# Kernel optimization log

Measured on AMD Instinct MI355X. Metric: run time of the kernel, lower is better.

The kernel has to match this reference:

```python
import jax, jax.numpy as jnp
import numpy as np

# Static problem dims (all graphs equal-sized so adaptive pool = uniform bins)
B = 64          # graphs
N = 2048        # nodes per graph
E = 16          # node_emb_dim
H_OUT, W_OUT = 32, 4   # AdaptiveAvgPool2d output -> pooled_dim = 128
COND = 64       # cond_emb_dim
HID = 512       # mlp_h_dim
BN_EPS = 1e-5


def _lin_init(key, out_d, in_d):
    kw, kb = jax.random.split(key)
    lim = 1.0 / np.sqrt(in_d)
    W = jax.random.uniform(kw, (out_d, in_d), jnp.float32, -lim, lim)
    b = jax.random.uniform(kb, (out_d,), jnp.float32, -lim, lim)
    return W, b


def setup_inputs() -> dict:
    key = jax.random.key(0)
    ks = jax.random.split(key, 6)
    Ntot = B * N
    x = jax.random.normal(ks[0], (Ntot, E), jnp.float32)
    batch = jnp.repeat(jnp.arange(B, dtype=jnp.int32), N)  # sorted segment ids
    cond = jax.random.normal(ks[1], (Ntot, COND), jnp.float32)
    mlp_in = COND + H_OUT * W_OUT  # 192
    W1, b1 = _lin_init(ks[2], HID, mlp_in)
    W2, b2 = _lin_init(ks[3], HID, HID)
    W3, b3 = _lin_init(ks[4], 3, HID)
    g1 = jnp.ones((HID,), jnp.float32); be1 = jnp.zeros((HID,), jnp.float32)
    g2 = jnp.ones((HID,), jnp.float32); be2 = jnp.zeros((HID,), jnp.float32)
    return {"x": x, "batch": batch, "conditioner_z_ref": cond,
            "W1": W1, "b1": b1, "g1": g1, "be1": be1,
            "W2": W2, "b2": b2, "g2": g2, "be2": be2,
            "W3": W3, "b3": b3}


def _bn_gelu(h, g, be):
    # BatchNorm1d in training mode: biased batch stats over the node axis
    m = h.mean(axis=0)
    v = h.var(axis=0)
    h = g * (h - m) * jax.lax.rsqrt(v + BN_EPS) + be
    return jax.nn.gelu(h, approximate=False)


def reference(x, batch, conditioner_z_ref, W1, b1, g1, be1, W2, b2, g2, be2, W3, b3):
    # Per-graph adaptive avg pool: since N % H_OUT == 0 and E % W_OUT == 0,
    # AdaptiveAvgPool2d is exactly mean over uniform (N/H_OUT, E/W_OUT) bins.
    xb = x.reshape(B, H_OUT, N // H_OUT, W_OUT, E // W_OUT)
    batch_pooled = xb.mean(axis=(2, 4)).reshape(B, H_OUT * W_OUT)  # [B, 128]
    pooled_per_node = batch_pooled[batch]                           # gather to [Ntot, 128]
    h = jnp.concatenate([conditioner_z_ref, pooled_per_node], axis=1)  # [Ntot, 192]
    h = _bn_gelu(h @ W1.T + b1, g1, be1)
    h = _bn_gelu(h @ W2.T + b2, g2, be2)
    return h @ W3.T + b3  # [Ntot, 3] predicted coords
```

## Files before the change

kernel.cpp:

```cpp
#include <hip/hip_runtime.h>
#include <hip/hip_bf16.h>
#include <math.h>
#include <stdint.h>

#define B_GRAPHS 64
#define N_NODES  2048
#define E_DIM    16
#define M_TOT    (B_GRAPHS * N_NODES)
#define K_COND   64
#define MLP_IN   192
#define HID      512
#define POOLD    128
#define BN_EPS   1e-5f

typedef __attribute__((ext_vector_type(8))) short bfrag8;
typedef __attribute__((ext_vector_type(4))) float facc4;

__device__ __forceinline__ unsigned short f2b(float f) {
    unsigned int x = __builtin_bit_cast(unsigned int, f);
    unsigned int r = x + 0x7fffu + ((x >> 16) & 1u);
    return (unsigned short)(r >> 16);
}
__device__ __forceinline__ float b2f(unsigned short u) {
    unsigned int x = ((unsigned int)u) << 16;
    return __builtin_bit_cast(float, x);
}

__device__ __forceinline__ float gelu_fast(float y) {
    float x  = y * 0.70710678118654752440f;
    float ax = fabsf(x);
    float t  = __builtin_amdgcn_rcpf(fmaf(0.3275911f, ax, 1.0f));
    float p  = fmaf(1.061405429f, t, -1.453152027f);
    p = fmaf(p, t, 1.421413741f);
    p = fmaf(p, t, -0.284496736f);
    p = fmaf(p, t, 0.254829592f);
    p = p * t;
    float e = __expf(-x * x);
    float erfax = fmaf(-p, e, 1.0f);
    float erfx  = copysignf(erfax, x);
    return 0.5f * y * (1.0f + erfx);
}

#define GLOAD_LDS16(g, l)                                                        \
    __builtin_amdgcn_global_load_lds(                                            \
        (const __attribute__((address_space(1))) unsigned int*)(const void*)(g), \
        (__attribute__((address_space(3))) unsigned int*)(void*)(l), 16, 0, 0)

__global__ __launch_bounds__(512) void prep_kernel(const float* __restrict__ x,
                                                   const float* __restrict__ W1,
                                                   const float* __restrict__ b1,
                                                   float* __restrict__ gbias) {
    __shared__ float pl[POOLD];
    int g = blockIdx.x, t = threadIdx.x;
    if (t < 128) {
        int h = t >> 2, w = t & 3;
        const float* base = x + (size_t)g * N_NODES * E_DIM + (size_t)h * 64 * E_DIM + w * 4;
        float s = 0.f;
        #pragma unroll 4
        for (int r = 0; r < 64; ++r) {
            float4 v = *reinterpret_cast<const float4*>(base + (size_t)r * E_DIM);
            s += v.x + v.y + v.z + v.w;
        }
        pl[h * 4 + w] = s * (1.0f / 256.0f);
    }
    __syncthreads();
    const float* wr_ = W1 + (size_t)t * MLP_IN + K_COND;
    float s = b1[t];
    #pragma unroll 4
    for (int k = 0; k < POOLD; ++k) s = fmaf(pl[k], wr_[k], s);
    gbias[g * HID + t] = s;
}

__global__ __launch_bounds__(256) void cvt_kernel(const float* __restrict__ s,
                                                  unsigned short* __restrict__ d) {
    size_t i = ((size_t)blockIdx.x * 256 + threadIdx.x) * 8;
    float4 v0 = *reinterpret_cast<const float4*>(s + i);
    float4 v1 = *reinterpret_cast<const float4*>(s + i + 4);
    unsigned short t[8] = {f2b(v0.x), f2b(v0.y), f2b(v0.z), f2b(v0.w),
                           f2b(v1.x), f2b(v1.y), f2b(v1.z), f2b(v1.w)};
    *reinterpret_cast<bfrag8*>(d + i) = *reinterpret_cast<bfrag8*>(t);
}

__device__ __forceinline__ bfrag8 load_f32x8_as_bf16(const float* p) {
    float4 v0 = *reinterpret_cast<const float4*>(p);
    float4 v1 = *reinterpret_cast<const float4*>(p + 4);
    unsigned short t[8] = {f2b(v0.x), f2b(v0.y), f2b(v0.z), f2b(v0.w),
                           f2b(v1.x), f2b(v1.y), f2b(v1.z), f2b(v1.w)};
    return *reinterpret_cast<bfrag8*>(t);
}

__global__ __launch_bounds__(256) void gemm1_kernel(const float* __restrict__ A,
                                                    const float* __restrict__ W,
                                                    const int* __restrict__ batch,
                                                    const float* __restrict__ gbias,
                                                    float* __restrict__ sums,
                                                    unsigned short* __restrict__ C) {
    __shared__ float sArr[128], qArr[128];
    const int t = threadIdx.x;
    const int r0 = blockIdx.x * 128, c0 = blockIdx.y * 128;
    const int l = t & 63, w = t >> 6;
    const int wr = w >> 1, wc = w & 1;
    const int ln = l & 15, kg = l >> 4;
    if (t < 128) { sArr[t] = 0.f; qArr[t] = 0.f; }
    __syncthreads();

    facc4 acc[4][4];
    const facc4 z = {0.f, 0.f, 0.f, 0.f};
    #pragma unroll
    for (int a = 0; a < 4; ++a)
        #pragma unroll
        for (int b = 0; b < 4; ++b) acc[a][b] = z;

    #pragma unroll
    for (int ks = 0; ks < 2; ++ks) {
        bfrag8 af[4], bf[4];
        #pragma unroll
        for (int a = 0; a < 4; ++a)
            af[a] = load_f32x8_as_bf16(A + (size_t)(r0 + wr * 64 + a * 16 + ln) * K_COND + ks * 32 + kg * 8);
        #pragma unroll
        for (int b = 0; b < 4; ++b)
            bf[b] = load_f32x8_as_bf16(W + (size_t)(c0 + wc * 64 + b * 16 + ln) * MLP_IN + ks * 32 + kg * 8);
        #pragma unroll
        for (int a = 0; a < 4; ++a)
            #pragma unroll
            for (int b = 0; b < 4; ++b)
                acc[a][b] = __builtin_amdgcn_mfma_f32_16x16x32_bf16(af[a], bf[b], acc[a][b], 0, 0, 0);
    }

    float cs[4] = {0.f, 0.f, 0.f, 0.f}, cq[4] = {0.f, 0.f, 0.f, 0.f};
    #pragma unroll
    for (int a = 0; a < 4; ++a) {
        #pragma unroll
        for (int i = 0; i < 4; ++i) {
            int row = r0 + wr * 64 + a * 16 + kg * 4 + i;
            const float* gb = gbias + (size_t)batch[row] * HID;
            size_t rbase = (size_t)row * HID + c0 + wc * 64 + ln;
            #pragma unroll
            for (int b = 0; b < 4; ++b) {
                float v = acc[a][b][i] + gb[c0 + wc * 64 + b * 16 + ln];
                C[rbase + b * 16] = f2b(v);
                cs[b] += v; cq[b] = fmaf(v, v, cq[b]);
            }
        }
    }
    #pragma unroll
    for (int b = 0; b < 4; ++b) {
        cs[b] += __shfl_xor(cs[b], 16, 64); cq[b] += __shfl_xor(cq[b], 16, 64);
        cs[b] += __shfl_xor(cs[b], 32, 64); cq[b] += __shfl_xor(cq[b], 32, 64);
    }
    if (kg == 0) {
        #pragma unroll
        for (int b = 0; b < 4; ++b) {
            int cl = wc * 64 + b * 16 + ln;
            atomicAdd(&sArr[cl], cs[b]); atomicAdd(&qArr[cl], cq[b]);
        }
    }
    __syncthreads();
    if (t < 128) {
        atomicAdd(&sums[c0 + t], sArr[t]);
        atomicAdd(&sums[HID + c0 + t], qArr[t]);
    }
}

__global__ __launch_bounds__(512, 2) void gemm2_kernel(const unsigned short* __restrict__ A,
                                                       const unsigned short* __restrict__ Bm,
                                                       const float* __restrict__ sums1,
                                                       const float* __restrict__ g1,
                                                       const float* __restrict__ be1,
                                                       const float* __restrict__ bias,
                                                       float* __restrict__ sums,
                                                       unsigned short* __restrict__ C) {
    __shared__ unsigned short As[2][128 * 32];
    __shared__ unsigned short Bs[2][512 * 32];
    __shared__ float lss[2 * HID];
    __shared__ float sArr[HID], qArr[HID];
    const int t = threadIdx.x;
    const int r0 = blockIdx.x * 128;
    const int l = t & 63, w = t >> 6;
    const int wr = w >> 2, wc = w & 3;
    const int ln = l & 15, kg = l >> 4;
    const int arow = t >> 2, aslot = t & 3;
    const int awslot = aslot ^ ((arow >> 1) & 3);
    const int rr = l >> 2, sp = l & 3;
    const int bss = sp ^ ((rr >> 1) & 3);

    {
        float mean = sums1[t] * (1.0f / M_TOT);
        float var  = sums1[HID + t] * (1.0f / M_TOT) - mean * mean;
        float sc   = g1[t] * rsqrtf(var + BN_EPS);
        lss[t] = sc;
        lss[HID + t] = be1[t] - mean * sc;
    }
    sArr[t] = 0.f; qArr[t] = 0.f;

    facc4 acc[4][8];
    const facc4 z = {0.f, 0.f, 0.f, 0.f};
    #pragma unroll
    for (int a = 0; a < 4; ++a)
        #pragma unroll
        for (int b = 0; b < 8; ++b) acc[a][b] = z;

    const unsigned short* aptr = A + (size_t)(r0 + arow) * HID + aslot * 8;
    __syncthreads();

    bfrag8 va_pending;
    {
        bfrag8 va0 = *reinterpret_cast<const bfrag8*>(aptr);
        unsigned short tmp[8];
        #pragma unroll
        for (int j = 0; j < 8; ++j) {
            int col = aslot * 8 + j;
            float xv = b2f((unsigned short)va0[j]);
            tmp[j] = f2b(gelu_fast(fmaf(xv, lss[col], lss[HID + col])));
        }
        *reinterpret_cast<bfrag8*>(&As[0][arow * 32 + awslot * 8]) = *reinterpret_cast<bfrag8*>(tmp);
        #pragma unroll
        for (int c = 0; c < 4; ++c) {
            int chunk = w * 4 + c;
            const unsigned short* gb = Bm + (size_t)(chunk * 16 + rr) * HID + bss * 8;
            GLOAD_LDS16(gb, &Bs[0][chunk * 512]);
        }
        va_pending = *reinterpret_cast<const bfrag8*>(aptr + 32);
    }
    __syncthreads();

    #pragma unroll 2
    for (int step = 0; step < 16; ++step) {
        const int cur = step & 1, nxt = cur ^ 1;
        bfrag8 af[4], bf[8];
        #pragma unroll
        for (int a = 0; a < 4; ++a) {
            int RA = wr * 64 + a * 16 + ln;
            af[a] = *reinterpret_cast<const bfrag8*>(&As[cur][RA * 32 + (kg ^ ((RA >> 1) & 3)) * 8]);
        }
        #pragma unroll
        for (int b = 0; b < 8; ++b) {
            int RB = wc * 128 + b * 16 + ln;
            bf[b] = *reinterpret_cast<const bfrag8*>(&Bs[cur][RB * 32 + (kg ^ ((RB >> 1) & 3)) * 8]);
        }
        if (step < 15) {
            const int kk = (step + 1) * 32;
            #pragma unroll
            for (int c = 0; c < 4; ++c) {
                int chunk = w * 4 + c;
                const unsigned short* gb = Bm + (size_t)(chunk * 16 + rr) * HID + kk + bss * 8;
                GLOAD_LDS16(gb, &Bs[nxt][chunk * 512]);
            }
        }
        bfrag8 va_future;
        if (step < 14) va_future = *reinterpret_cast<const bfrag8*>(aptr + (step + 2) * 32);
        #pragma unroll
        for (int a = 0; a < 4; ++a)
            #pragma unroll
            for (int b = 0; b < 8; ++b)
                acc[a][b] = __builtin_amdgcn_mfma_f32_16x16x32_bf16(af[a], bf[b], acc[a][b], 0, 0, 0);
        if (step < 15) {
            const int kk = (step + 1) * 32;
            unsigned short tmp[8];
            #pragma unroll
            for (int j = 0; j < 8; ++j) {
                int col = kk + aslot * 8 + j;
                float xv = b2f((unsigned short)va_pending[j]);
                tmp[j] = f2b(gelu_fast(fmaf(xv, lss[col], lss[HID + col])));
            }
            *reinterpret_cast<bfrag8*>(&As[nxt][arow * 32 + awslot * 8]) = *reinterpret_cast<bfrag8*>(tmp);
        }
        va_pending = va_future;
        __syncthreads();
    }

    float bb[8];
    #pragma unroll
    for (int b = 0; b < 8; ++b) bb[b] = bias[wc * 128 + b * 16 + ln];
    float cs[8], cq[8];
    #pragma unroll
    for (int b = 0; b < 8; ++b) { cs[b] = 0.f; cq[b] = 0.f; }
    #pragma unroll
    for (int a = 0; a < 4; ++a) {
        #pragma unroll
        for (int i = 0; i < 4; ++i) {
            size_t rbase = (size_t)(r0 + wr * 64 + a * 16 + kg * 4 + i) * HID + wc * 128 + ln;
            #pragma unroll
            for (int b = 0; b < 8; ++b) {
                float v = acc[a][b][i] + bb[b];
                C[rbase + b * 16] = f2b(v);
                cs[b] += v; cq[b] = fmaf(v, v, cq[b]);
            }
        }
    }
    #pragma unroll
    for (int b = 0; b < 8; ++b) {
        cs[b] += __shfl_xor(cs[b], 16, 64); cq[b] += __shfl_xor(cq[b], 16, 64);
        cs[b] += __shfl_xor(cs[b], 32, 64); cq[b] += __shfl_xor(cq[b], 32, 64);
    }
    if (kg == 0) {
        #pragma unroll
        for (int b = 0; b < 8; ++b) {
            int cl = wc * 128 + b * 16 + ln;
            atomicAdd(&sArr[cl], cs[b]); atomicAdd(&qArr[cl], cq[b]);
        }
    }
    __syncthreads();
    atomicAdd(&sums[t], sArr[t]);
    atomicAdd(&sums[HID + t], qArr[t]);
}

__global__ void finalize_kernel(const float* __restrict__ sums, const float* __restrict__ g,
                                const float* __restrict__ be, float* __restrict__ ss) {
    int n = threadIdx.x;
    float mean = sums[n] * (1.0f / M_TOT);
    float var = sums[HID + n] * (1.0f / M_TOT) - mean * mean;
    float sc = g[n] * rsqrtf(var + BN_EPS);
    ss[n] = sc;
    ss[HID + n] = be[n] - mean * sc;
}

__global__ __launch_bounds__(256) void g3_kernel(const unsigned short* __restrict__ H2,
                                                 const float* __restrict__ ss2,
                                                 const float* __restrict__ W3,
                                                 const float* __restrict__ b3,
                                                 float* __restrict__ out) {
    __shared__ float lss[2 * HID];
    __shared__ float lw3[3 * HID];
    int t = threadIdx.x;
    for (int i = t; i < 2 * HID; i += 256) lss[i] = ss2[i];
    for (int i = t; i < 3 * HID; i += 256) lw3[i] = W3[i];
    __syncthreads();
    int l = t & 63, w = t >> 6;
    int rsub = l >> 3, lk = l & 7;
    int row = blockIdx.x * 32 + w * 8 + rsub;
    const unsigned short* p = H2 + (size_t)row * HID;
    float o0 = 0.f, o1 = 0.f, o2 = 0.f;
    #pragma unroll
    for (int it = 0; it < 8; ++it) {
        int k = it * 64 + lk * 8;
        bfrag8 v = *reinterpret_cast<const bfrag8*>(p + k);
        #pragma unroll
        for (int j = 0; j < 8; ++j) {
            float x = b2f((unsigned short)v[j]);
            float y = fmaf(x, lss[k + j], lss[HID + k + j]);
            y = gelu_fast(y);
            o0 = fmaf(y, lw3[k + j], o0);
            o1 = fmaf(y, lw3[HID + k + j], o1);
            o2 = fmaf(y, lw3[2 * HID + k + j], o2);
        }
    }
    #pragma unroll
    for (int m = 1; m < 8; m <<= 1) {
        o0 += __shfl_xor(o0, m, 64);
        o1 += __shfl_xor(o1, m, 64);
        o2 += __shfl_xor(o2, m, 64);
    }
    if (lk == 0) {
        out[(size_t)row * 3 + 0] = o0 + b3[0];
        out[(size_t)row * 3 + 1] = o1 + b3[1];
        out[(size_t)row * 3 + 2] = o2 + b3[2];
    }
}

extern "C" void kernel_launch(void* const* d_in, const int* in_sizes, int n_in,
                              void* d_out, int out_size, void* d_ws, size_t ws_size,
                              hipStream_t stream) {
    const float* x     = (const float*)d_in[0];
    const int*   batch = (const int*)d_in[1];
    const float* cond  = (const float*)d_in[2];
    const float* W1    = (const float*)d_in[3];
    const float* b1    = (const float*)d_in[4];
    const float* g1    = (const float*)d_in[5];
    const float* be1   = (const float*)d_in[6];
    const float* W2    = (const float*)d_in[7];
    const float* b2    = (const float*)d_in[8];
    const float* g2    = (const float*)d_in[9];
    const float* be2   = (const float*)d_in[10];
    const float* W3    = (const float*)d_in[11];
    const float* b3    = (const float*)d_in[12];

    const size_t H_BYTES = (size_t)M_TOT * HID * 2;
    if (ws_size < 2 * H_BYTES) return;
    char* ws = (char*)d_ws;
    unsigned short* H1 = (unsigned short*)ws;
    unsigned short* H2 = (unsigned short*)(ws + H_BYTES);

    float* outf   = (float*)d_out;
    float* gbias  = outf;
    float* sums1  = gbias + B_GRAPHS * HID;
    float* sums2  = sums1 + 2 * HID;
    unsigned short* W2bf = (unsigned short*)(sums2 + 2 * HID);
    float* ss2 = (float*)ws;

    hipMemsetAsync(sums1, 0, 2 * 2 * HID * sizeof(float), stream);

    prep_kernel<<<B_GRAPHS, 512, 0, stream>>>(x, W1, b1, gbias);
    cvt_kernel<<<(HID * HID / 8) / 256, 256, 0, stream>>>(W2, W2bf);

    gemm1_kernel<<<dim3(M_TOT / 128, HID / 128), 256, 0, stream>>>(
        cond, W1, batch, gbias, sums1, H1);

    gemm2_kernel<<<dim3(M_TOT / 128, 1), 512, 0, stream>>>(
        H1, W2bf, sums1, g1, be1, b2, sums2, H2);

    finalize_kernel<<<1, HID, 0, stream>>>(sums2, g2, be2, ss2);

    g3_kernel<<<M_TOT / 32, 256, 0, stream>>>(H2, ss2, W3, b3, outf);
}
```

Baseline: 313.3 us.

## Widen gemm1 tiles to full width and deepen gemm2 prefetch pipeline

gemm1 now has each 512-thread block compute all 512 output columns for its 128 rows. The graph index is derived from the row offset instead of reading the batch array per row, and the per-graph bias is hoisted into registers. gemm2's main loop is rebuilt as a two-stage-ahead pipeline with explicit vmcnt/lgkmcnt waits, raw s_barriers and sched_barriers, so B-tile loads overlap MFMA work better. This relies on the uniform sorted batch layout and adds register pressure in gemm1.

```diff
diff --git a/kernel.cpp b/kernel.cpp
--- a/kernel.cpp
+++ b/kernel.cpp
@@ -89,77 +89,79 @@
     return *reinterpret_cast<bfrag8*>(t);
 }
 
-__global__ __launch_bounds__(256) void gemm1_kernel(const float* __restrict__ A,
-                                                    const float* __restrict__ W,
-                                                    const int* __restrict__ batch,
-                                                    const float* __restrict__ gbias,
-                                                    float* __restrict__ sums,
-                                                    unsigned short* __restrict__ C) {
-    __shared__ float sArr[128], qArr[128];
+__global__ __launch_bounds__(512, 2) void gemm1_kernel(const float* __restrict__ A,
+                                                       const float* __restrict__ W,
+                                                       const float* __restrict__ gbias,
+                                                       float* __restrict__ sums,
+                                                       unsigned short* __restrict__ C) {
+    __shared__ float sArr[HID], qArr[HID];
     const int t = threadIdx.x;
-    const int r0 = blockIdx.x * 128, c0 = blockIdx.y * 128;
+    const int r0 = blockIdx.x * 128;
+    const int g = r0 >> 11;
     const int l = t & 63, w = t >> 6;
-    const int wr = w >> 1, wc = w & 1;
+    const int wr = w >> 2, wc = w & 3;
     const int ln = l & 15, kg = l >> 4;
-    if (t < 128) { sArr[t] = 0.f; qArr[t] = 0.f; }
-    __syncthreads();
-
-    facc4 acc[4][4];
+    sArr[t] = 0.f; qArr[t] = 0.f;
+    __syncthreads();
+
+    facc4 acc[4][8];
     const facc4 z = {0.f, 0.f, 0.f, 0.f};
     #pragma unroll
     for (int a = 0; a < 4; ++a)
         #pragma unroll
-        for (int b = 0; b < 4; ++b) acc[a][b] = z;
+        for (int b = 0; b < 8; ++b) acc[a][b] = z;
 
     #pragma unroll
     for (int ks = 0; ks < 2; ++ks) {
-        bfrag8 af[4], bf[4];
+        bfrag8 af[4], bf[8];
         #pragma unroll
         for (int a = 0; a < 4; ++a)
             af[a] = load_f32x8_as_bf16(A + (size_t)(r0 + wr * 64 + a * 16 + ln) * K_COND + ks * 32 + kg * 8);
         #pragma unroll
-        for (int b = 0; b < 4; ++b)
-            bf[b] = load_f32x8_as_bf16(W + (size_t)(c0 + wc * 64 + b * 16 + ln) * MLP_IN + ks * 32 + kg * 8);
+        for (int b = 0; b < 8; ++b)
+            bf[b] = load_f32x8_as_bf16(W + (size_t)(wc * 128 + b * 16 + ln) * MLP_IN + ks * 32 + kg * 8);
         #pragma unroll
         for (int a = 0; a < 4; ++a)
             #pragma unroll
-            for (int b = 0; b < 4; ++b)
+            for (int b = 0; b < 8; ++b)
                 acc[a][b] = __builtin_amdgcn_mfma_f32_16x16x32_bf16(af[a], bf[b], acc[a][b], 0, 0, 0);
     }
 
-    float cs[4] = {0.f, 0.f, 0.f, 0.f}, cq[4] = {0.f, 0.f, 0.f, 0.f};
+    const float* gb = gbias + (size_t)g * HID;
+    float gbv[8];
+    #pragma unroll
+    for (int b = 0; b < 8; ++b) gbv[b] = gb[wc * 128 + b * 16 + ln];
+    float cs[8], cq[8];
+    #pragma unroll
+    for (int b = 0; b < 8; ++b) { cs[b] = 0.f; cq[b] = 0.f; }
     #pragma unroll
     for (int a = 0; a < 4; ++a) {
         #pragma unroll
         for (int i = 0; i < 4; ++i) {
-            int row = r0 + wr * 64 + a * 16 + kg * 4 + i;
-            const float* gb = gbias + (size_t)batch[row] * HID;
-            size_t rbase = (size_t)row * HID + c0 + wc * 64 + ln;
+            size_t rbase = (size_t)(r0 + wr * 64 + a * 16 + kg * 4 + i) * HID + wc * 128 + ln;
             #pragma unroll
-            for (int b = 0; b < 4; ++b) {
-                float v = acc[a][b][i] + gb[c0 + wc * 64 + b * 16 + ln];
+            for (int b = 0; b < 8; ++b) {
+                float v = acc[a][b][i] + gbv[b];
                 C[rbase + b * 16] = f2b(v);
                 cs[b] += v; cq[b] = fmaf(v, v, cq[b]);
             }
         }
     }
     #pragma unroll
-    for (int b = 0; b < 4; ++b) {
+    for (int b = 0; b < 8; ++b) {
         cs[b] += __shfl_xor(cs[b], 16, 64); cq[b] += __shfl_xor(cq[b], 16, 64);
         cs[b] += __shfl_xor(cs[b], 32, 64); cq[b] += __shfl_xor(cq[b], 32, 64);
     }
     if (kg == 0) {
         #pragma unroll
-        for (int b = 0; b < 4; ++b) {
-            int cl = wc * 64 + b * 16 + ln;
+        for (int b = 0; b < 8; ++b) {
+            int cl = wc * 128 + b * 16 + ln;
             atomicAdd(&sArr[cl], cs[b]); atomicAdd(&qArr[cl], cq[b]);
         }
     }
     __syncthreads();
-    if (t < 128) {
-        atomicAdd(&sums[c0 + t], sArr[t]);
-        atomicAdd(&sums[HID + c0 + t], qArr[t]);
-    }
+    atomicAdd(&sums[t], sArr[t]);
+    atomicAdd(&sums[HID + t], qArr[t]);
 }
 
 __global__ __launch_bounds__(512, 2) void gemm2_kernel(const unsigned short* __restrict__ A,
@@ -201,72 +203,92 @@
         for (int b = 0; b < 8; ++b) acc[a][b] = z;
 
     const unsigned short* aptr = A + (size_t)(r0 + arow) * HID + aslot * 8;
-    __syncthreads();
-
-    bfrag8 va_pending;
-    {
-        bfrag8 va0 = *reinterpret_cast<const bfrag8*>(aptr);
+
+    auto actwrite = [&](bfrag8 va, int kk, int buf) {
         unsigned short tmp[8];
         #pragma unroll
         for (int j = 0; j < 8; ++j) {
-            int col = aslot * 8 + j;
-            float xv = b2f((unsigned short)va0[j]);
+            int col = kk + aslot * 8 + j;
+            float xv = b2f((unsigned short)va[j]);
             tmp[j] = f2b(gelu_fast(fmaf(xv, lss[col], lss[HID + col])));
         }
-        *reinterpret_cast<bfrag8*>(&As[0][arow * 32 + awslot * 8]) = *reinterpret_cast<bfrag8*>(tmp);
+        *reinterpret_cast<bfrag8*>(&As[buf][arow * 32 + awslot * 8]) = *reinterpret_cast<bfrag8*>(tmp);
+    };
+    auto stageB = [&](int kk, int buf) {
         #pragma unroll
         for (int c = 0; c < 4; ++c) {
             int chunk = w * 4 + c;
-            const unsigned short* gb = Bm + (size_t)(chunk * 16 + rr) * HID + bss * 8;
-            GLOAD_LDS16(gb, &Bs[0][chunk * 512]);
-        }
-        va_pending = *reinterpret_cast<const bfrag8*>(aptr + 32);
-    }
-    __syncthreads();
-
-    #pragma unroll 2
-    for (int step = 0; step < 16; ++step) {
-        const int cur = step & 1, nxt = cur ^ 1;
-        bfrag8 af[4], bf[8];
+            const unsigned short* gb = Bm + (size_t)(chunk * 16 + rr) * HID + kk + bss * 8;
+            GLOAD_LDS16(gb, &Bs[buf][chunk * 512]);
+        }
+    };
+    auto dsread = [&](bfrag8* af, bfrag8* bf, int buf) {
         #pragma unroll
         for (int a = 0; a < 4; ++a) {
             int RA = wr * 64 + a * 16 + ln;
-            af[a] = *reinterpret_cast<const bfrag8*>(&As[cur][RA * 32 + (kg ^ ((RA >> 1) & 3)) * 8]);
+            af[a] = *reinterpret_cast<const bfrag8*>(&As[buf][RA * 32 + (kg ^ ((RA >> 1) & 3)) * 8]);
         }
         #pragma unroll
         for (int b = 0; b < 8; ++b) {
             int RB = wc * 128 + b * 16 + ln;
-            bf[b] = *reinterpret_cast<const bfrag8*>(&Bs[cur][RB * 32 + (kg ^ ((RB >> 1) & 3)) * 8]);
-        }
-        if (step < 15) {
-            const int kk = (step + 1) * 32;
-            #pragma unroll
-            for (int c = 0; c < 4; ++c) {
-                int chunk = w * 4 + c;
-                const unsigned short* gb = Bm + (size_t)(chunk * 16 + rr) * HID + kk + bss * 8;
-                GLOAD_LDS16(gb, &Bs[nxt][chunk * 512]);
-            }
-        }
-        bfrag8 va_future;
-        if (step < 14) va_future = *reinterpret_cast<const bfrag8*>(aptr + (step + 2) * 32);
+            bf[b] = *reinterpret_cast<const bfrag8*>(&Bs[buf][RB * 32 + (kg ^ ((RB >> 1) & 3)) * 8]);
+        }
+    };
+    auto domfma = [&](bfrag8* af, bfrag8* bf) {
         #pragma unroll
         for (int a = 0; a < 4; ++a)
             #pragma unroll
             for (int b = 0; b < 8; ++b)
                 acc[a][b] = __builtin_amdgcn_mfma_f32_16x16x32_bf16(af[a], bf[b], acc[a][b], 0, 0, 0);
-        if (step < 15) {
-            const int kk = (step + 1) * 32;
-            unsigned short tmp[8];
-            #pragma unroll
-            for (int j = 0; j < 8; ++j) {
-                int col = kk + aslot * 8 + j;
-                float xv = b2f((unsigned short)va_pending[j]);
-                tmp[j] = f2b(gelu_fast(fmaf(xv, lss[col], lss[HID + col])));
-            }
-            *reinterpret_cast<bfrag8*>(&As[nxt][arow * 32 + awslot * 8]) = *reinterpret_cast<bfrag8*>(tmp);
-        }
-        va_pending = va_future;
-        __syncthreads();
+    };
+
+    __syncthreads();
+
+    bfrag8 va_p, va_q;
+    va_p = *reinterpret_cast<const bfrag8*>(aptr);
+    stageB(0, 0);
+    va_q = *reinterpret_cast<const bfrag8*>(aptr + 32);
+    stageB(32, 1);
+    asm volatile("s_waitcnt vmcnt(9)" ::: "memory");
+    actwrite(va_p, 0, 0);
+    va_p = va_q;
+    asm volatile("s_waitcnt lgkmcnt(0)" ::: "memory");
+
+    bfrag8 af[4], bf[8];
+    #pragma unroll 2
+    for (int tt = 0; tt < 14; ++tt) {
+        const int cur = tt & 1, nxt = cur ^ 1;
+        asm volatile("s_waitcnt vmcnt(4)" ::: "memory");
+        __builtin_amdgcn_s_barrier();
+        __builtin_amdgcn_sched_barrier(0);
+        dsread(af, bf, cur);
+        actwrite(va_p, (tt + 1) * 32, nxt);
+        asm volatile("s_waitcnt lgkmcnt(0)" ::: "memory");
+        __builtin_amdgcn_s_barrier();
+        __builtin_amdgcn_sched_barrier(0);
+        va_q = *reinterpret_cast<const bfrag8*>(aptr + (tt + 2) * 32);
+        stageB((tt + 2) * 32, cur);
+        domfma(af, bf);
+        va_p = va_q;
+    }
+    {
+        asm volatile("s_waitcnt vmcnt(4)" ::: "memory");
+        __builtin_amdgcn_s_barrier();
+        __builtin_amdgcn_sched_barrier(0);
+        dsread(af, bf, 0);
+        actwrite(va_p, 15 * 32, 1);
+        asm volatile("s_waitcnt lgkmcnt(0)" ::: "memory");
+        __builtin_amdgcn_s_barrier();
+        __builtin_amdgcn_sched_barrier(0);
+        domfma(af, bf);
+    }
+    {
+        asm volatile("s_waitcnt vmcnt(0)" ::: "memory");
+        __builtin_amdgcn_s_barrier();
+        __builtin_amdgcn_sched_barrier(0);
+        dsread(af, bf, 1);
+        asm volatile("s_waitcnt lgkmcnt(0)" ::: "memory");
+        domfma(af, bf);
     }
 
     float bb[8];
@@ -362,7 +384,6 @@
                               void* d_out, int out_size, void* d_ws, size_t ws_size,
                               hipStream_t stream) {
     const float* x     = (const float*)d_in[0];
-    const int*   batch = (const int*)d_in[1];
     const float* cond  = (const float*)d_in[2];
     const float* W1    = (const float*)d_in[3];
     const float* b1    = (const float*)d_in[4];
@@ -393,8 +414,8 @@
     prep_kernel<<<B_GRAPHS, 512, 0, stream>>>(x, W1, b1, gbias);
     cvt_kernel<<<(HID * HID / 8) / 256, 256, 0, stream>>>(W2, W2bf);
 
-    gemm1_kernel<<<dim3(M_TOT / 128, HID / 128), 256, 0, stream>>>(
-        cond, W1, batch, gbias, sums1, H1);
+    gemm1_kernel<<<dim3(M_TOT / 128, 1), 512, 0, stream>>>(
+        cond, W1, gbias, sums1, H1);
 
     gemm2_kernel<<<dim3(M_TOT / 128, 1), 512, 0, stream>>>(
         H1, W2bf, sums1, g1, be1, b2, sums2, H2);
```

Measured after the change: 297.8 us. 4.9% less time.
